# Optimization experiments

Measured on AMD Instinct MI355X. Metric: run time of the kernel, lower is better.

## Reference

```python
import jax, jax.numpy as jnp
import numpy as np

KH = KW = 3
STRIDE = 1
ITERATIONS = 2
EPS = 1e-7


def _squash(s):
    # squash along last axis (capsule dim)
    sn = jnp.sum(s * s, axis=-1, keepdims=True)
    return (sn / (1.0 + sn)) * s / jnp.sqrt(sn + EPS)


def setup_inputs() -> dict:
    key = jax.random.key(0)
    k1, k2 = jax.random.split(key)
    x = jax.random.normal(k1, (4, 14, 14, 32, 8), dtype=jnp.float32)
    # W: [1,1,1,filters_out, caps_per_patch=3*3*32, dims_out=16, dims_in=8], stddev=0.1 init
    W = 0.1 * jax.random.normal(k2, (1, 1, 1, 32, 288, 16, 8), dtype=jnp.float32)
    return {"x": x, "W": W}


def reference(x, W):
    B, H, Wd, Fin, Din = x.shape
    Ho = (H - KH) // STRIDE + 1
    Wo = (Wd - KW) // STRIDE + 1
    # Patch extraction, channel order (kh, kw, Fin) to match tf.image.extract_patches
    patches = jnp.stack(
        [x[:, i:i + Ho * STRIDE:STRIDE, j:j + Wo * STRIDE:STRIDE]
         for i in range(KH) for j in range(KW)],
        axis=3,
    )  # [B,Ho,Wo,KH*KW,Fin,Din]
    patches = patches.reshape(B, Ho, Wo, KH * KW * Fin, Din)  # [B,Ho,Wo,C,Di]

    Wm = W[0, 0, 0]  # [F, C, Do, Di]
    F, C, Do, _ = Wm.shape
    # predictions[b,h,w,f,c,o] = sum_i W[f,c,o,i] * patches[b,h,w,c,i]
    preds = jnp.einsum('fcoi,bhwci->bhwfco', Wm, patches)

    logits = jnp.zeros((B, Ho, Wo, F, C), dtype=preds.dtype)
    outputs = jnp.zeros((B, Ho, Wo, F, Do), dtype=preds.dtype)
    for _ in range(ITERATIONS):
        # agreement = predictions^T @ outputs over the dims_out axis
        agreement = jnp.einsum('bhwfco,bhwfo->bhwfc', preds, outputs)
        logits = logits + agreement
        # NOTE: original code softmaxes over axis=3 (the filters_out axis)
        cc = jax.nn.softmax(logits, axis=3)  # [B,Ho,Wo,F,C]
        centroids = jnp.sum(cc[..., None] * preds, axis=4)  # [B,Ho,Wo,F,Do]
        outputs = _squash(centroids)
    return outputs
```

## Files before the change

kernel.cpp:

```cpp
#include <hip/hip_runtime.h>

#define NB   4
#define H_IN 14
#define W_IN 14
#define FIN  32
#define DI   8
#define F    32
#define C    288
#define DO   16
#define HO   12
#define WO   12
#define NPOS (NB*HO*WO)
#define EPS  1e-7f

#define CH   16
#define CC   (C/CH)
#define GP   2
#define GRID2 ((CH*NPOS/GP)/4)

#define KTOT (C*DI)
#define KPAD 2312

#define W2H_BYTES  ((size_t)F*C*DO*DI*2)
#define WH_BYTES   ((size_t)F*C*DO*DI*2)
#define PH_BYTES   ((size_t)NPOS*KTOT*2)
#define PART_BYTES ((size_t)CH*NPOS*F*DO*4)
#define OUT1_BYTES ((size_t)NPOS*F*DO*4)

#define CVT_W2H 576
#define CVT_WH  576
#define CVT_PH  648
#define CVT_GRID (CVT_W2H + CVT_WH + CVT_PH)

typedef _Float16 h2 __attribute__((ext_vector_type(2)));
typedef _Float16 h8v __attribute__((ext_vector_type(8)));
typedef float    f4v __attribute__((ext_vector_type(4)));

__device__ __forceinline__ unsigned int pack2(float a, float b) {
    h2 v; v.x = (_Float16)a; v.y = (_Float16)b;
    return __builtin_bit_cast(unsigned int, v);
}

__device__ __forceinline__ float dot8h(const uint4 w, const uint4 v, float acc) {
#if __has_builtin(__builtin_amdgcn_fdot2)
    acc = __builtin_amdgcn_fdot2(__builtin_bit_cast(h2, w.x), __builtin_bit_cast(h2, v.x), acc, false);
    acc = __builtin_amdgcn_fdot2(__builtin_bit_cast(h2, w.y), __builtin_bit_cast(h2, v.y), acc, false);
    acc = __builtin_amdgcn_fdot2(__builtin_bit_cast(h2, w.z), __builtin_bit_cast(h2, v.z), acc, false);
    acc = __builtin_amdgcn_fdot2(__builtin_bit_cast(h2, w.w), __builtin_bit_cast(h2, v.w), acc, false);
#else
    const h2 w0 = __builtin_bit_cast(h2, w.x), v0 = __builtin_bit_cast(h2, v.x);
    const h2 w1 = __builtin_bit_cast(h2, w.y), v1 = __builtin_bit_cast(h2, v.y);
    const h2 w2 = __builtin_bit_cast(h2, w.z), v2 = __builtin_bit_cast(h2, v.z);
    const h2 w3 = __builtin_bit_cast(h2, w.w), v3 = __builtin_bit_cast(h2, v.w);
    acc += (float)w0.x*(float)v0.x + (float)w0.y*(float)v0.y
         + (float)w1.x*(float)v1.x + (float)w1.y*(float)v1.y
         + (float)w2.x*(float)v2.x + (float)w2.y*(float)v2.y
         + (float)w3.x*(float)v3.x + (float)w3.y*(float)v3.y;
#endif
    return acc;
}

__device__ __forceinline__ int xbase_of(int pos) {
    const int b = pos/(HO*WO), rem = pos%(HO*WO), ho = rem/WO, wo = rem%WO;
    return ((b*H_IN + ho)*W_IN + wo)*FIN*DI;
}

__device__ __forceinline__ int coff_of(int c) {
    const int slab = c >> 5, fin = c & 31;
    const int kh = slab/3, kw = slab%3;
    return (kh*W_IN + kw)*FIN*DI + fin*DI;
}

__global__ __launch_bounds__(256) void kernConv(const float* __restrict__ Wt,
                                                const float* __restrict__ x,
                                                unsigned short* __restrict__ W2h,
                                                unsigned short* __restrict__ Wh,
                                                unsigned short* __restrict__ Ph) {
    const int b = blockIdx.x;
    if (b < CVT_W2H) {
        const int idx = b*256 + threadIdx.x;
        const float* src = Wt + (size_t)idx*8;
        const float4 a = *(const float4*)src;
        const float4 bb = *(const float4*)(src + 4);
        uint4 r;
        r.x = pack2(a.x, a.y);   r.y = pack2(a.z, a.w);
        r.z = pack2(bb.x, bb.y); r.w = pack2(bb.z, bb.w);
        const int o = idx & 15;
        const int c = (idx >> 4) % C;
        const int f = idx / (C*DO);
        ((uint4*)W2h)[(size_t)(c*DO + o)*F + f] = r;
    } else if (b < CVT_W2H + CVT_WH) {
        const int idx = (b - CVT_W2H)*256 + threadIdx.x;
        const float* src = Wt + (size_t)idx*8;
        const float4 a = *(const float4*)src;
        const float4 bb = *(const float4*)(src + 4);
        uint4 r;
        r.x = pack2(a.x, a.y);   r.y = pack2(a.z, a.w);
        r.z = pack2(bb.x, bb.y); r.w = pack2(bb.z, bb.w);
        ((uint4*)Wh)[idx] = r;
    } else {
        const int pc = (b - CVT_W2H - CVT_WH)*256 + threadIdx.x;
        const int pos = pc / C, c = pc % C;
        const float* src = x + xbase_of(pos) + coff_of(c);
        const float4 a = *(const float4*)src;
        const float4 bb = *(const float4*)(src + 4);
        uint4 r;
        r.x = pack2(a.x, a.y);   r.y = pack2(a.z, a.w);
        r.z = pack2(bb.x, bb.y); r.w = pack2(bb.z, bb.w);
        ((uint4*)Ph)[pc] = r;
    }
}

__global__ __launch_bounds__(512) void kernM1(const unsigned short* __restrict__ Ph,
                                              const unsigned short* __restrict__ Wh,
                                              float* __restrict__ out1)
{
    __shared__ unsigned short As[16][KPAD];
    __shared__ f4v red2[4][64];

    const int tid  = threadIdx.x;
    const int lane = tid & 63;
    const int wv   = tid >> 6;
    const int pt   = blockIdx.x >> 3;
    const int fg   = blockIdx.x & 7;
    const int f    = (wv & 3)*8 + fg;
    const int ks   = wv >> 2;
    const int pos0 = pt*16;
    const int n    = lane & 15, q = lane >> 4;

    #pragma unroll
    for (int r = 0; r < 9; ++r) {
        const int linear = r*512 + tid;
        const int row = linear / 288, col8 = linear % 288;
        const uint4 v = *(const uint4*)(Ph + (size_t)(pos0 + row)*KTOT + col8*8);
        *(uint4*)&As[row][col8*8] = v;
    }
    __syncthreads();

    const unsigned short* pa = &As[n][q*8];
    const unsigned short* pb = Wh + ((size_t)(f*C + q)*DO + n)*DI;

    f4v acc0 = {0.f,0.f,0.f,0.f}, acc1 = {0.f,0.f,0.f,0.f};
    const int s0 = ks*36;
    #pragma unroll 4
    for (int s = s0; s < s0 + 36; s += 2) {
        const h8v a0 = *(const h8v*)(pa + s*32);
        const h8v b0 = *(const h8v*)(pb + (size_t)s*4*DO*DI);
        const h8v a1 = *(const h8v*)(pa + (s+1)*32);
        const h8v b1 = *(const h8v*)(pb + (size_t)(s+1)*4*DO*DI);
        acc0 = __builtin_amdgcn_mfma_f32_16x16x32_f16(a0, b0, acc0, 0, 0, 0);
        acc1 = __builtin_amdgcn_mfma_f32_16x16x32_f16(a1, b1, acc1, 0, 0, 0);
    }

    f4v tot;
    #pragma unroll
    for (int r = 0; r < 4; ++r) tot[r] = acc0[r] + acc1[r];

    if (wv >= 4) red2[wv - 4][lane] = tot;
    __syncthreads();

    if (wv < 4) {
        const f4v other = red2[wv][lane];
        #pragma unroll
        for (int r = 0; r < 4; ++r) {
            const float v = (tot[r] + other[r]) * (1.f/32.f);
            float sq = v*v;
            sq += __shfl_xor(sq, 1);
            sq += __shfl_xor(sq, 2);
            sq += __shfl_xor(sq, 4);
            sq += __shfl_xor(sq, 8);
            const float sc = (sq/(1.f + sq)) * rsqrtf(sq + EPS);
            out1[(size_t)(pos0 + q*4 + r)*512 + f*DO + n] = v * sc;
        }
    }
}

__global__ __launch_bounds__(256) void kern2w(const unsigned short* __restrict__ Ph,
                                              const unsigned short* __restrict__ W2h,
                                              const float* __restrict__ out1,
                                              float* __restrict__ part2)
{
    __shared__ uint4 Ws[2][512];

    const int tid  = threadIdx.x;
    const int lane = tid & 63;
    const int wv   = tid >> 6;
    const int f    = lane & 31;
    const int og   = lane >> 5;
    const int o0   = og*8;

    const int ch   = blockIdx.x & (CH-1);
    const int gq   = blockIdx.x >> 4;
    const int grp  = __builtin_amdgcn_readfirstlane(gq*4 + wv);
    const int pos0 = grp*GP;

    const int c0 = ch*CC;
    const uint4* W2h4 = (const uint4*)W2h;

    float u[8][GP];
    #pragma unroll
    for (int p = 0; p < GP; ++p) {
        const float* up = out1 + (size_t)(pos0 + p)*512 + f*DO + o0;
        const float4 a = *(const float4*)up;
        const float4 b = *(const float4*)(up + 4);
        u[0][p]=a.x; u[1][p]=a.y; u[2][p]=a.z; u[3][p]=a.w;
        u[4][p]=b.x; u[5][p]=b.y; u[6][p]=b.z; u[7][p]=b.w;
    }

    float acc[8][GP];
    #pragma unroll
    for (int k = 0; k < 8; ++k)
        #pragma unroll
        for (int p = 0; p < GP; ++p) acc[k][p] = 0.f;

    Ws[0][tid]       = W2h4[(size_t)c0*512 + tid];
    Ws[0][tid + 256] = W2h4[(size_t)c0*512 + tid + 256];

    #pragma unroll 1
    for (int cl = 0; cl < CC; ++cl) {
        __syncthreads();
        const int buf = cl & 1;
        if (cl + 1 < CC) {
            const size_t cb = (size_t)(c0 + cl + 1)*512;
            Ws[buf^1][tid]       = W2h4[cb + tid];
            Ws[buf^1][tid + 256] = W2h4[cb + tid + 256];
        }
        const int c = c0 + cl;

        uint4 xv[GP];
        #pragma unroll
        for (int p = 0; p < GP; ++p)
            xv[p] = *(const uint4*)(Ph + (size_t)(pos0 + p)*KTOT + c*DI);

        float pred[8][GP];
        #pragma unroll
        for (int k = 0; k < 8; ++k) {
            const uint4 w = Ws[buf][(o0 + k)*32 + f];
            #pragma unroll
            for (int p = 0; p < GP; ++p) pred[k][p] = dot8h(w, xv[p], 0.f);
        }

        #pragma unroll
        for (int p = 0; p < GP; ++p) {
            float ap = 0.f;
            #pragma unroll
            for (int k = 0; k < 8; ++k) ap += pred[k][p]*u[k][p];
            ap += __shfl_xor(ap, 32);

            float m = ap;
            m = fmaxf(m, __shfl_xor(m, 1));
            m = fmaxf(m, __shfl_xor(m, 2));
            m = fmaxf(m, __shfl_xor(m, 4));
            m = fmaxf(m, __shfl_xor(m, 8));
            m = fmaxf(m, __shfl_xor(m, 16));
            const float e = __expf(ap - m);
            float s = e;
            s += __shfl_xor(s, 1);
            s += __shfl_xor(s, 2);
            s += __shfl_xor(s, 4);
            s += __shfl_xor(s, 8);
            s += __shfl_xor(s, 16);
            const float cc = e / s;

            #pragma unroll
            for (int k = 0; k < 8; ++k) acc[k][p] += cc*pred[k][p];
        }
    }

    #pragma unroll
    for (int p = 0; p < GP; ++p) {
        float* dst = part2 + ((size_t)(ch*NPOS + pos0 + p)*F + f)*DO + o0;
        float4 s0, s1;
        s0.x=acc[0][p]; s0.y=acc[1][p]; s0.z=acc[2][p]; s0.w=acc[3][p];
        s1.x=acc[4][p]; s1.y=acc[5][p]; s1.z=acc[6][p]; s1.w=acc[7][p];
        *(float4*)dst = s0;
        *(float4*)(dst + 4) = s1;
    }
}

__global__ __launch_bounds__(64) void kern3(const float* __restrict__ part2,
                                            float* __restrict__ out)
{
    const int lane = threadIdx.x;
    const int pos  = blockIdx.x;
    const int f = lane & 31, oh = lane >> 5, o0 = oh*8;

    float c0x=0.f,c0y=0.f,c0z=0.f,c0w=0.f, c1x=0.f,c1y=0.f,c1z=0.f,c1w=0.f;
    #pragma unroll
    for (int k = 0; k < CH; ++k) {
        const float* s = part2 + ((size_t)(k*NPOS + pos)*F + f)*DO + o0;
        const float4 a = *(const float4*)s;
        const float4 b = *(const float4*)(s + 4);
        c0x+=a.x; c0y+=a.y; c0z+=a.z; c0w+=a.w;
        c1x+=b.x; c1y+=b.y; c1z+=b.z; c1w+=b.w;
    }
    float sq = c0x*c0x + c0y*c0y + c0z*c0z + c0w*c0w
             + c1x*c1x + c1y*c1y + c1z*c1z + c1w*c1w;
    sq += __shfl_xor(sq, 32);
    const float sc = (sq/(1.f + sq)) * rsqrtf(sq + EPS);

    float* dst = out + ((size_t)pos*F + f)*DO + o0;
    float4 s0, s1;
    s0.x=c0x*sc; s0.y=c0y*sc; s0.z=c0z*sc; s0.w=c0w*sc;
    s1.x=c1x*sc; s1.y=c1y*sc; s1.z=c1z*sc; s1.w=c1w*sc;
    *(float4*)dst = s0;
    *(float4*)(dst + 4) = s1;
}

__device__ __forceinline__ float dot8(const float4* __restrict__ w,
                                      const float4 p0, const float4 p1) {
    float4 a = w[0], b = w[1];
    return a.x*p0.x + a.y*p0.y + a.z*p0.z + a.w*p0.w
         + b.x*p1.x + b.y*p1.y + b.z*p1.z + b.w*p1.w;
}

__global__ __launch_bounds__(256) void capsule_kernel_f32(
    const float* __restrict__ x, const float* __restrict__ Wt,
    float* __restrict__ out)
{
    __shared__ float patch[C*DI];
    __shared__ float cent[F*DO];
    __shared__ float out1[F*DO];
    __shared__ float agr[F*C];
    __shared__ float scale_s[F];

    const int tid = threadIdx.x;
    const int pos = blockIdx.x;
    const int b   = pos / (HO*WO);
    const int rem = pos % (HO*WO);
    const int ho  = rem / WO;
    const int wo  = rem % WO;

    #pragma unroll
    for (int slab = 0; slab < 9; ++slab) {
        const int kh = slab / 3, kw = slab % 3;
        const float* src = x + (((b*H_IN + ho + kh)*W_IN + (wo + kw))*FIN)*DI;
        patch[slab*256 + tid] = src[tid];
    }
    __syncthreads();

    const float4* pv = (const float4*)patch;

    {
        const int fo0 = tid, fo1 = tid + 256;
        const int f0 = fo0 >> 4, o0 = fo0 & 15;
        const int f1 = fo1 >> 4, o1 = fo1 & 15;
        float acc0 = 0.f, acc1 = 0.f;
        for (int c = 0; c < C; ++c) {
            const float4 p0 = pv[c*2], p1 = pv[c*2+1];
            acc0 += dot8((const float4*)(Wt + ((f0*C + c)*DO + o0)*DI), p0, p1);
            acc1 += dot8((const float4*)(Wt + ((f1*C + c)*DO + o1)*DI), p0, p1);
        }
        cent[fo0] = acc0 * (1.f/32.f);
        cent[fo1] = acc1 * (1.f/32.f);
    }
    __syncthreads();

    if (tid < F) {
        float sn = 0.f;
        #pragma unroll
        for (int o = 0; o < DO; ++o) { float v = cent[tid*DO + o]; sn += v*v; }
        const float sc = (sn/(1.f + sn)) * rsqrtf(sn + EPS);
        #pragma unroll
        for (int o = 0; o < DO; ++o) out1[tid*DO + o] = cent[tid*DO + o] * sc;
    }
    __syncthreads();

    #pragma unroll 1
    for (int r = 0; r < (F*C)/256; ++r) {
        const int pp = tid + 256*r;
        const int f = pp / C, c = pp % C;
        const float4* wrow = (const float4*)(Wt + (f*C + c)*DO*DI);
        const float4 p0 = pv[c*2], p1 = pv[c*2+1];
        float a = 0.f;
        #pragma unroll
        for (int o = 0; o < DO; ++o) a += dot8(wrow + o*2, p0, p1) * out1[f*DO + o];
        agr[pp] = a;
    }
    __syncthreads();

    for (int c = tid; c < C; c += 256) {
        float m = -1e30f;
        #pragma unroll
        for (int f = 0; f < F; ++f) m = fmaxf(m, agr[f*C + c]);
        float s = 0.f;
        #pragma unroll
        for (int f = 0; f < F; ++f) {
            const float e = __expf(agr[f*C + c] - m);
            agr[f*C + c] = e; s += e;
        }
        const float inv = 1.f / s;
        #pragma unroll
        for (int f = 0; f < F; ++f) agr[f*C + c] *= inv;
    }
    __syncthreads();

    {
        const int fo0 = tid, fo1 = tid + 256;
        const int f0 = fo0 >> 4, o0 = fo0 & 15;
        const int f1 = fo1 >> 4, o1 = fo1 & 15;
        float acc0 = 0.f, acc1 = 0.f;
        for (int c = 0; c < C; ++c) {
            const float4 p0 = pv[c*2], p1 = pv[c*2+1];
            acc0 += agr[f0*C + c] * dot8((const float4*)(Wt + ((f0*C + c)*DO + o0)*DI), p0, p1);
            acc1 += agr[f1*C + c] * dot8((const float4*)(Wt + ((f1*C + c)*DO + o1)*DI), p0, p1);
        }
        cent[fo0] = acc0;
        cent[fo1] = acc1;
    }
    __syncthreads();

    if (tid < F) {
        float sn = 0.f;
        #pragma unroll
        for (int o = 0; o < DO; ++o) { float v = cent[tid*DO + o]; sn += v*v; }
        scale_s[tid] = (sn/(1.f + sn)) * rsqrtf(sn + EPS);
    }
    __syncthreads();

    out[pos*(F*DO) + tid]       = cent[tid]       * scale_s[tid >> 4];
    out[pos*(F*DO) + tid + 256] = cent[tid + 256] * scale_s[(tid >> 4) + 16];
}

extern "C" void kernel_launch(void* const* d_in, const int* in_sizes, int n_in,
                              void* d_out, int out_size, void* d_ws, size_t ws_size,
                              hipStream_t stream) {
    const float* x  = (const float*)d_in[0];
    const float* Wt = (const float*)d_in[1];
    float* out = (float*)d_out;

    if (ws_size >= W2H_BYTES + WH_BYTES + PH_BYTES + PART_BYTES + OUT1_BYTES) {
        char* p = (char*)d_ws;
        unsigned short* W2h = (unsigned short*)p;            p += W2H_BYTES;
        unsigned short* Wh  = (unsigned short*)p;            p += WH_BYTES;
        unsigned short* Ph  = (unsigned short*)p;            p += PH_BYTES;
        float* part = (float*)p;                             p += PART_BYTES;
        float* out1 = (float*)p;

        kernConv<<<CVT_GRID, 256, 0, stream>>>(Wt, x, W2h, Wh, Ph);
        kernM1<<<36*8, 512, 0, stream>>>(Ph, Wh, out1);
        kern2w<<<GRID2, 256, 0, stream>>>(Ph, W2h, out1, part);
        kern3<<<NPOS, 64, 0, stream>>>(part, out);
    } else {
        capsule_kernel_f32<<<NPOS, 256, 0, stream>>>(x, Wt, out);
    }
}
```

Baseline: 125.0 us.

## Split capsule channels across half-waves and read weights directly from global memory

The second routing kernel no longer stages weights in double-buffered shared memory with block barriers. Each half-wave now handles a different input capsule and computes all 16 output dims, reading its weights straight from global memory (via cache), and the two halves' partial sums are merged by a cross-lane shuffle at the end. This removes the per-iteration __syncthreads and LDS traffic, and it adds a launch-bounds occupancy hint. In exchange it doubles per-thread registers for u/acc/pred and relies on cache hits for weight reuse across waves.

```diff
diff --git a/kernel.cpp b/kernel.cpp
--- a/kernel.cpp
+++ b/kernel.cpp
@@ -175,77 +175,60 @@
     }
 }
 
-__global__ __launch_bounds__(256) void kern2w(const unsigned short* __restrict__ Ph,
-                                              const unsigned short* __restrict__ W2h,
-                                              const float* __restrict__ out1,
-                                              float* __restrict__ part2)
+__global__ __launch_bounds__(256, 4) void kern2w(const unsigned short* __restrict__ Ph,
+                                                 const unsigned short* __restrict__ W2h,
+                                                 const float* __restrict__ out1,
+                                                 float* __restrict__ part2)
 {
-    __shared__ uint4 Ws[2][512];
-
     const int tid  = threadIdx.x;
     const int lane = tid & 63;
     const int wv   = tid >> 6;
     const int f    = lane & 31;
     const int og   = lane >> 5;
-    const int o0   = og*8;
 
     const int ch   = blockIdx.x & (CH-1);
     const int gq   = blockIdx.x >> 4;
-    const int grp  = __builtin_amdgcn_readfirstlane(gq*4 + wv);
-    const int pos0 = grp*GP;
+    const int pos0 = (gq*4 + wv)*GP;
 
     const int c0 = ch*CC;
     const uint4* W2h4 = (const uint4*)W2h;
 
-    float u[8][GP];
+    float u[16][GP];
     #pragma unroll
     for (int p = 0; p < GP; ++p) {
-        const float* up = out1 + (size_t)(pos0 + p)*512 + f*DO + o0;
-        const float4 a = *(const float4*)up;
-        const float4 b = *(const float4*)(up + 4);
-        u[0][p]=a.x; u[1][p]=a.y; u[2][p]=a.z; u[3][p]=a.w;
-        u[4][p]=b.x; u[5][p]=b.y; u[6][p]=b.z; u[7][p]=b.w;
-    }
-
-    float acc[8][GP];
-    #pragma unroll
-    for (int k = 0; k < 8; ++k)
-        #pragma unroll
-        for (int p = 0; p < GP; ++p) acc[k][p] = 0.f;
-
-    Ws[0][tid]       = W2h4[(size_t)c0*512 + tid];
-    Ws[0][tid + 256] = W2h4[(size_t)c0*512 + tid + 256];
+        const float4* up = (const float4*)(out1 + (size_t)(pos0 + p)*512 + f*DO);
+        const float4 a = up[0], b = up[1], cq = up[2], d = up[3];
+        u[0][p]=a.x;  u[1][p]=a.y;  u[2][p]=a.z;  u[3][p]=a.w;
+        u[4][p]=b.x;  u[5][p]=b.y;  u[6][p]=b.z;  u[7][p]=b.w;
+        u[8][p]=cq.x; u[9][p]=cq.y; u[10][p]=cq.z; u[11][p]=cq.w;
+        u[12][p]=d.x; u[13][p]=d.y; u[14][p]=d.z; u[15][p]=d.w;
+    }
+
+    float acc[16][GP];
+    #pragma unroll
+    for (int o = 0; o < 16; ++o)
+        #pragma unroll
+        for (int p = 0; p < GP; ++p) acc[o][p] = 0.f;
 
     #pragma unroll 1
-    for (int cl = 0; cl < CC; ++cl) {
-        __syncthreads();
-        const int buf = cl & 1;
-        if (cl + 1 < CC) {
-            const size_t cb = (size_t)(c0 + cl + 1)*512;
-            Ws[buf^1][tid]       = W2h4[cb + tid];
-            Ws[buf^1][tid + 256] = W2h4[cb + tid + 256];
-        }
-        const int c = c0 + cl;
-
-        uint4 xv[GP];
-        #pragma unroll
-        for (int p = 0; p < GP; ++p)
-            xv[p] = *(const uint4*)(Ph + (size_t)(pos0 + p)*KTOT + c*DI);
-
-        float pred[8][GP];
-        #pragma unroll
-        for (int k = 0; k < 8; ++k) {
-            const uint4 w = Ws[buf][(o0 + k)*32 + f];
+    for (int st = 0; st < CC/2; ++st) {
+        const int c = c0 + st*2 + og;
+        const uint4* wbase = W2h4 + (size_t)c*DO*F + f;
+
+        #pragma unroll
+        for (int p = 0; p < GP; ++p) {
+            const uint4 xv = *(const uint4*)(Ph + (size_t)(pos0 + p)*KTOT + c*DI);
+
+            float pred[16];
             #pragma unroll
-            for (int p = 0; p < GP; ++p) pred[k][p] = dot8h(w, xv[p], 0.f);
-        }
-
-        #pragma unroll
-        for (int p = 0; p < GP; ++p) {
+            for (int o = 0; o < 16; ++o) {
+                const uint4 w = wbase[o*F];
+                pred[o] = dot8h(w, xv, 0.f);
+            }
+
             float ap = 0.f;
             #pragma unroll
-            for (int k = 0; k < 8; ++k) ap += pred[k][p]*u[k][p];
-            ap += __shfl_xor(ap, 32);
+            for (int o = 0; o < 16; ++o) ap += pred[o]*u[o][p];
 
             float m = ap;
             m = fmaxf(m, __shfl_xor(m, 1));
@@ -260,19 +243,31 @@
             s += __shfl_xor(s, 4);
             s += __shfl_xor(s, 8);
             s += __shfl_xor(s, 16);
-            const float cc = e / s;
+            const float cw = e / s;
 
             #pragma unroll
-            for (int k = 0; k < 8; ++k) acc[k][p] += cc*pred[k][p];
+            for (int o = 0; o < 16; ++o) acc[o][p] += cw*pred[o];
         }
     }
 
     #pragma unroll
     for (int p = 0; p < GP; ++p) {
-        float* dst = part2 + ((size_t)(ch*NPOS + pos0 + p)*F + f)*DO + o0;
+        #pragma unroll
+        for (int o = 0; o < 16; ++o) acc[o][p] += __shfl_xor(acc[o][p], 32);
+
+        const float v0 = og ? acc[8][p]  : acc[0][p];
+        const float v1 = og ? acc[9][p]  : acc[1][p];
+        const float v2 = og ? acc[10][p] : acc[2][p];
+        const float v3 = og ? acc[11][p] : acc[3][p];
+        const float v4 = og ? acc[12][p] : acc[4][p];
+        const float v5 = og ? acc[13][p] : acc[5][p];
+        const float v6 = og ? acc[14][p] : acc[6][p];
+        const float v7 = og ? acc[15][p] : acc[7][p];
+
+        float* dst = part2 + ((size_t)(ch*NPOS + pos0 + p)*F + f)*DO + og*8;
         float4 s0, s1;
-        s0.x=acc[0][p]; s0.y=acc[1][p]; s0.z=acc[2][p]; s0.w=acc[3][p];
-        s1.x=acc[4][p]; s1.y=acc[5][p]; s1.z=acc[6][p]; s1.w=acc[7][p];
+        s0.x=v0; s0.y=v1; s0.z=v2; s0.w=v3;
+        s1.x=v4; s1.y=v5; s1.z=v6; s1.w=v7;
         *(float4*)dst = s0;
         *(float4*)(dst + 4) = s1;
     }
```

Result: slower. 157.7 us (+26.2%).

## Split first-iteration GEMM across blocks, defer squash, drop LDS staging and softmax max

Applied to the files above, without the earlier changes.

The first-iteration MFMA kernel now splits the K dimension across two 256-thread blocks instead of two wave groups inside one 512-thread block. It writes two partial outputs, and the next kernel sums them, scales and squashes them on load. The routing kernel drops its double-buffered LDS staging of W2h and the barriers that came with it, reading weights directly from global memory and caches. It also removes the max-subtraction in the softmax, which trades numerical safety for fewer shuffles and relies on the logits staying small enough not to overflow.

```diff
diff --git a/kernel.cpp b/kernel.cpp
--- a/kernel.cpp
+++ b/kernel.cpp
@@ -18,14 +18,15 @@
 #define GP   2
 #define GRID2 ((CH*NPOS/GP)/4)
 
-#define KTOT (C*DI)
-#define KPAD 2312
+#define KTOT  (C*DI)
+#define KHALF 1152
+#define KPADH 1156
 
 #define W2H_BYTES  ((size_t)F*C*DO*DI*2)
 #define WH_BYTES   ((size_t)F*C*DO*DI*2)
 #define PH_BYTES   ((size_t)NPOS*KTOT*2)
 #define PART_BYTES ((size_t)CH*NPOS*F*DO*4)
-#define OUT1_BYTES ((size_t)NPOS*F*DO*4)
+#define OUT1P_BYTES ((size_t)2*NPOS*F*DO*4)
 
 #define CVT_W2H 576
 #define CVT_WH  576
@@ -111,39 +112,37 @@
     }
 }
 
-__global__ __launch_bounds__(512) void kernM1(const unsigned short* __restrict__ Ph,
+__global__ __launch_bounds__(256) void kernM1(const unsigned short* __restrict__ Ph,
                                               const unsigned short* __restrict__ Wh,
-                                              float* __restrict__ out1)
+                                              float* __restrict__ out1p)
 {
-    __shared__ unsigned short As[16][KPAD];
-    __shared__ f4v red2[4][64];
+    __shared__ unsigned short As[16][KPADH];
 
     const int tid  = threadIdx.x;
     const int lane = tid & 63;
     const int wv   = tid >> 6;
-    const int pt   = blockIdx.x >> 3;
-    const int fg   = blockIdx.x & 7;
-    const int f    = (wv & 3)*8 + fg;
-    const int ks   = wv >> 2;
+    const int ks   = blockIdx.x & 1;
+    const int fg   = (blockIdx.x >> 1) & 7;
+    const int pt   = blockIdx.x >> 4;
+    const int f    = wv*8 + fg;
     const int pos0 = pt*16;
     const int n    = lane & 15, q = lane >> 4;
 
     #pragma unroll
     for (int r = 0; r < 9; ++r) {
-        const int linear = r*512 + tid;
-        const int row = linear / 288, col8 = linear % 288;
-        const uint4 v = *(const uint4*)(Ph + (size_t)(pos0 + row)*KTOT + col8*8);
-        *(uint4*)&As[row][col8*8] = v;
+        const int linear = r*256 + tid;
+        const int row = linear / 144, col = linear % 144;
+        const uint4 v = *(const uint4*)(Ph + (size_t)(pos0 + row)*KTOT + ks*KHALF + col*8);
+        *(uint4*)&As[row][col*8] = v;
     }
     __syncthreads();
 
     const unsigned short* pa = &As[n][q*8];
-    const unsigned short* pb = Wh + ((size_t)(f*C + q)*DO + n)*DI;
+    const unsigned short* pb = Wh + ((size_t)(f*C + ks*144 + q)*DO + n)*DI;
 
     f4v acc0 = {0.f,0.f,0.f,0.f}, acc1 = {0.f,0.f,0.f,0.f};
-    const int s0 = ks*36;
     #pragma unroll 4
-    for (int s = s0; s < s0 + 36; s += 2) {
+    for (int s = 0; s < 36; s += 2) {
         const h8v a0 = *(const h8v*)(pa + s*32);
         const h8v b0 = *(const h8v*)(pb + (size_t)s*4*DO*DI);
         const h8v a1 = *(const h8v*)(pa + (s+1)*32);
@@ -152,36 +151,17 @@
         acc1 = __builtin_amdgcn_mfma_f32_16x16x32_f16(a1, b1, acc1, 0, 0, 0);
     }
 
-    f4v tot;
-    #pragma unroll
-    for (int r = 0; r < 4; ++r) tot[r] = acc0[r] + acc1[r];
-
-    if (wv >= 4) red2[wv - 4][lane] = tot;
-    __syncthreads();
-
-    if (wv < 4) {
-        const f4v other = red2[wv][lane];
-        #pragma unroll
-        for (int r = 0; r < 4; ++r) {
-            const float v = (tot[r] + other[r]) * (1.f/32.f);
-            float sq = v*v;
-            sq += __shfl_xor(sq, 1);
-            sq += __shfl_xor(sq, 2);
-            sq += __shfl_xor(sq, 4);
-            sq += __shfl_xor(sq, 8);
-            const float sc = (sq/(1.f + sq)) * rsqrtf(sq + EPS);
-            out1[(size_t)(pos0 + q*4 + r)*512 + f*DO + n] = v * sc;
-        }
+    #pragma unroll
+    for (int r = 0; r < 4; ++r) {
+        out1p[((size_t)ks*NPOS + pos0 + q*4 + r)*512 + f*DO + n] = acc0[r] + acc1[r];
     }
 }
 
 __global__ __launch_bounds__(256) void kern2w(const unsigned short* __restrict__ Ph,
                                               const unsigned short* __restrict__ W2h,
-                                              const float* __restrict__ out1,
+                                              const float* __restrict__ out1p,
                                               float* __restrict__ part2)
 {
-    __shared__ uint4 Ws[2][512];
-
     const int tid  = threadIdx.x;
     const int lane = tid & 63;
     const int wv   = tid >> 6;
@@ -200,11 +180,24 @@
     float u[8][GP];
     #pragma unroll
     for (int p = 0; p < GP; ++p) {
-        const float* up = out1 + (size_t)(pos0 + p)*512 + f*DO + o0;
-        const float4 a = *(const float4*)up;
-        const float4 b = *(const float4*)(up + 4);
-        u[0][p]=a.x; u[1][p]=a.y; u[2][p]=a.z; u[3][p]=a.w;
-        u[4][p]=b.x; u[5][p]=b.y; u[6][p]=b.z; u[7][p]=b.w;
+        const float* up0 = out1p + (size_t)(pos0 + p)*512 + f*DO + o0;
+        const float* up1 = up0 + (size_t)NPOS*512;
+        const float4 a0 = *(const float4*)up0;
+        const float4 b0 = *(const float4*)(up0 + 4);
+        const float4 a1 = *(const float4*)up1;
+        const float4 b1 = *(const float4*)(up1 + 4);
+        float ur[8];
+        ur[0]=(a0.x+a1.x)*(1.f/32.f); ur[1]=(a0.y+a1.y)*(1.f/32.f);
+        ur[2]=(a0.z+a1.z)*(1.f/32.f); ur[3]=(a0.w+a1.w)*(1.f/32.f);
+        ur[4]=(b0.x+b1.x)*(1.f/32.f); ur[5]=(b0.y+b1.y)*(1.f/32.f);
+        ur[6]=(b0.z+b1.z)*(1.f/32.f); ur[7]=(b0.w+b1.w)*(1.f/32.f);
+        float sq = 0.f;
+        #pragma unroll
+        for (int k = 0; k < 8; ++k) sq += ur[k]*ur[k];
+        sq += __shfl_xor(sq, 32);
+        const float sc = (sq/(1.f + sq)) * rsqrtf(sq + EPS);
+        #pragma unroll
+        for (int k = 0; k < 8; ++k) u[k][p] = ur[k]*sc;
     }
 
     float acc[8][GP];
@@ -212,19 +205,9 @@
     for (int k = 0; k < 8; ++k)
         #pragma unroll
         for (int p = 0; p < GP; ++p) acc[k][p] = 0.f;
-
-    Ws[0][tid]       = W2h4[(size_t)c0*512 + tid];
-    Ws[0][tid + 256] = W2h4[(size_t)c0*512 + tid + 256];
 
     #pragma unroll 1
     for (int cl = 0; cl < CC; ++cl) {
-        __syncthreads();
-        const int buf = cl & 1;
-        if (cl + 1 < CC) {
-            const size_t cb = (size_t)(c0 + cl + 1)*512;
-            Ws[buf^1][tid]       = W2h4[cb + tid];
-            Ws[buf^1][tid + 256] = W2h4[cb + tid + 256];
-        }
         const int c = c0 + cl;
 
         uint4 xv[GP];
@@ -235,7 +218,7 @@
         float pred[8][GP];
         #pragma unroll
         for (int k = 0; k < 8; ++k) {
-            const uint4 w = Ws[buf][(o0 + k)*32 + f];
+            const uint4 w = W2h4[(size_t)(c*DO + o0 + k)*F + f];
             #pragma unroll
             for (int p = 0; p < GP; ++p) pred[k][p] = dot8h(w, xv[p], 0.f);
         }
@@ -247,13 +230,7 @@
             for (int k = 0; k < 8; ++k) ap += pred[k][p]*u[k][p];
             ap += __shfl_xor(ap, 32);
 
-            float m = ap;
-            m = fmaxf(m, __shfl_xor(m, 1));
-            m = fmaxf(m, __shfl_xor(m, 2));
-            m = fmaxf(m, __shfl_xor(m, 4));
-            m = fmaxf(m, __shfl_xor(m, 8));
-            m = fmaxf(m, __shfl_xor(m, 16));
-            const float e = __expf(ap - m);
+            const float e = __expf(ap);
             float s = e;
             s += __shfl_xor(s, 1);
             s += __shfl_xor(s, 2);
@@ -429,17 +406,17 @@
     const float* Wt = (const float*)d_in[1];
     float* out = (float*)d_out;
 
-    if (ws_size >= W2H_BYTES + WH_BYTES + PH_BYTES + PART_BYTES + OUT1_BYTES) {
+    if (ws_size >= W2H_BYTES + WH_BYTES + PH_BYTES + PART_BYTES + OUT1P_BYTES) {
         char* p = (char*)d_ws;
         unsigned short* W2h = (unsigned short*)p;            p += W2H_BYTES;
         unsigned short* Wh  = (unsigned short*)p;            p += WH_BYTES;
         unsigned short* Ph  = (unsigned short*)p;            p += PH_BYTES;
         float* part = (float*)p;                             p += PART_BYTES;
-        float* out1 = (float*)p;
+        float* out1p = (float*)p;
 
         kernConv<<<CVT_GRID, 256, 0, stream>>>(Wt, x, W2h, Wh, Ph);
-        kernM1<<<36*8, 512, 0, stream>>>(Ph, Wh, out1);
-        kern2w<<<GRID2, 256, 0, stream>>>(Ph, W2h, out1, part);
+        kernM1<<<36*8*2, 256, 0, stream>>>(Ph, Wh, out1p);
+        kern2w<<<GRID2, 256, 0, stream>>>(Ph, W2h, out1p, part);
         kern3<<<NPOS, 64, 0, stream>>>(part, out);
     } else {
         capsule_kernel_f32<<<NPOS, 256, 0, stream>>>(x, Wt, out);
```

Measured after the change: 124.5 us. Within noise of the previous version (-0.4%).
